# Kernel optimization log

Hardware: AMD Instinct MI355X
Metric: run time of the kernel (lower is better)

The kernel has to match this reference:

```python
import jax, jax.numpy as jnp
import numpy as np

B, T, H, S, A, E = 256, 64, 2048, 512, 64, 2048


def setup_inputs() -> dict:
    key = jax.random.key(0)
    ks = jax.random.split(key, 16)
    def w(k, shape, fan_in):
        return (jax.random.normal(k, shape, dtype=jnp.float32) / np.float32(np.sqrt(fan_in)))
    return {
        "prev_hidden": jax.random.normal(ks[0], (B, H), dtype=jnp.float32),
        "prev_state": jax.random.normal(ks[1], (B, S), dtype=jnp.float32),
        "actions": jax.random.normal(ks[2], (B, T, A), dtype=jnp.float32),
        "obs": jax.random.normal(ks[3], (B, T, E), dtype=jnp.float32),
        "prior_noise": jax.random.normal(ks[4], (B, T - 1, S), dtype=jnp.float32),
        "post_noise": jax.random.normal(ks[5], (B, T - 1, S), dtype=jnp.float32),
        # project_state_action: Linear(A+S -> H), stored [in, out]
        "W_sa": w(ks[6], (S + A, H), S + A), "b_sa": jnp.zeros((H,), jnp.float32),
        # GRUCell weights in torch layout [3H, in]
        "W_ih": w(ks[7], (3 * H, H), H), "W_hh": w(ks[8], (3 * H, H), H),
        "b_ih": jnp.zeros((3 * H,), jnp.float32), "b_hh": jnp.zeros((3 * H,), jnp.float32),
        # project_hidden_action: Linear(H+A -> H)
        "W_ha": w(ks[9], (H + A, H), H + A), "b_ha": jnp.zeros((H,), jnp.float32),
        # prior: Linear(H -> 2S)
        "W_prior": w(ks[10], (H, 2 * S), H), "b_prior": jnp.zeros((2 * S,), jnp.float32),
        # project_hidden_obs: Linear(H+E -> H)
        "W_ho": w(ks[11], (H + E, H), H + E), "b_ho": jnp.zeros((H,), jnp.float32),
        # posterior: Linear(H -> 2S)
        "W_post": w(ks[12], (H, 2 * S), H), "b_post": jnp.zeros((2 * S,), jnp.float32),
        "stop": 0,
    }


def reference(prev_hidden, prev_state, actions, obs, prior_noise, post_noise,
              W_sa, b_sa, W_ih, W_hh, b_ih, b_hh, W_ha, b_ha,
              W_prior, b_prior, W_ho, b_ho, W_post, b_post, stop):
    relu = jax.nn.relu

    def gru(x, h):
        gi = x @ W_ih.T + b_ih  # [B, 3H]
        gh = h @ W_hh.T + b_hh
        ir, iz, inn = jnp.split(gi, 3, axis=-1)
        hr, hz, hn = jnp.split(gh, 3, axis=-1)
        r = jax.nn.sigmoid(ir + hr)
        z = jax.nn.sigmoid(iz + hz)
        n = jnp.tanh(inn + r * hn)
        return (1.0 - z) * n + z * h

    def step(carry, xs):
        h, s = carry  # h: [B,H] hidden, s: [B,S] posterior state (obs is given)
        a, o, pn, qn = xs
        sa = relu(jnp.concatenate([s, a], axis=-1) @ W_sa + b_sa)
        h = gru(sa, h)
        ha = relu(jnp.concatenate([h, a], axis=-1) @ W_ha + b_ha)
        pm, plv = jnp.split(ha @ W_prior + b_prior, 2, axis=-1)
        ps = pm + jnp.exp(jax.nn.softplus(plv)) * pn  # prior rsample
        ho = relu(jnp.concatenate([h, o], axis=-1) @ W_ho + b_ho)
        qm, qlv = jnp.split(ho @ W_post + b_post, 2, axis=-1)
        qs = qm + jnp.exp(jax.nn.softplus(qlv)) * qn  # posterior rsample
        return (h, qs), (h, ps, qs, pm, plv, qm, qlv)

    Tm1 = actions.shape[1] - 1
    xs = (jnp.swapaxes(actions[:, :Tm1], 0, 1),
          jnp.swapaxes(obs[:, :Tm1], 0, 1),
          jnp.swapaxes(prior_noise, 0, 1),
          jnp.swapaxes(post_noise, 0, 1))
    _, ys = jax.lax.scan(step, (prev_hidden, prev_state), xs)
    hs, ps, qs, pm, plv, qm, qlv = (jnp.swapaxes(y, 0, 1) for y in ys)
    hiddens = jnp.concatenate([prev_hidden[:, None, :], hs], axis=1)       # [B, T, H]
    prior_states = jnp.concatenate([prev_state[:, None, :], ps], axis=1)   # [B, T, S]
    posterior_states = jnp.concatenate([prev_state[:, None, :], qs], axis=1)
    return (hiddens, prior_states, posterior_states, pm, plv, qm, qlv)
```

## Files before the change

kernel.cpp:

```cpp
#include <hip/hip_runtime.h>


typedef __attribute__((ext_vector_type(8))) short bf16x8;
typedef __attribute__((ext_vector_type(4))) float f32x4;
typedef __attribute__((ext_vector_type(4))) short s16x4;

#define DEVI static __device__ __forceinline__

DEVI float bf2f(short s) { union { float f; unsigned u; } v; v.u = ((unsigned)(unsigned short)s) << 16; return v.f; }
DEVI short f2bf(float f) {
  union { float f; unsigned u; } v; v.f = f;
  unsigned r = v.u + 0x7FFFu + ((v.u >> 16) & 1u);
  return (short)(r >> 16);
}

#define Bsz 256
#define Tsz 64
#define Hsz 2048
#define Ssz 512
#define Asz 64
#define Esz 2048
#define TM1 63

#define OUT_PS  33554432L
#define OUT_QS  41943040L
#define OUT_PM  50331648L
#define OUT_PLV 58589184L
#define OUT_QM  66846720L
#define OUT_QLV 75104256L

struct GArg {
  const short* A; const short* Bt; const float* bias; const short* Ci;
  float* oF; short* oB;
  int lda, ldb, ldoF, ldoB; long ldci, pstride;
};

template<int HASBIAS, int HASCI, int RELU, int OUTF, int OUTB>
__global__ __launch_bounds__(256) void gemm_bt(GArg g0, GArg g1, int kcK) {
  const int gemm = blockIdx.z & 1;
  const GArg g = gemm ? g1 : g0;
  const short* __restrict__ Ag = g.A;
  const short* __restrict__ Bg = g.Bt;
  __shared__ __align__(16) short As[2][8192];
  __shared__ __align__(16) short Bs[2][8192];
  const int tid = threadIdx.x;
  const int w = tid >> 6, l = tid & 63;
  const int bm0 = blockIdx.y << 7, bn0 = blockIdx.x << 7;
  const int fc = l & 15, fh = l >> 4;
  const int wr = (w >> 1) << 6, wc = (w & 1) << 6;
  const int rx = fc & 7;
  const int srccol = ((l & 7) ^ ((l >> 3) & 7)) << 3;
  long aoff[4], boff[4];
#pragma unroll
  for (int i = 0; i < 4; ++i) {
    const int row = (((i << 2) + w) << 3) + (l >> 3);
    aoff[i] = (long)(bm0 + row) * g.lda + srccol;
    boff[i] = (long)(bn0 + row) * g.ldb + srccol;
  }
  f32x4 acc[4][4];
#pragma unroll
  for (int i = 0; i < 4; ++i)
#pragma unroll
    for (int j = 0; j < 4; ++j) acc[i][j] = f32x4{0.f, 0.f, 0.f, 0.f};

  auto STAGE = [&](int kt, int buf) {
#pragma unroll
    for (int i = 0; i < 4; ++i) {
      const int ib = ((i << 2) + w) << 10;
      __builtin_amdgcn_global_load_lds(
          (const __attribute__((address_space(1))) void*)(Ag + aoff[i] + (kt << 6)),
          (__attribute__((address_space(3))) void*)((char*)&As[buf][0] + ib), 16, 0, 0);
      __builtin_amdgcn_global_load_lds(
          (const __attribute__((address_space(1))) void*)(Bg + boff[i] + (kt << 6)),
          (__attribute__((address_space(3))) void*)((char*)&Bs[buf][0] + ib), 16, 0, 0);
    }
  };
  auto COMPUTE = [&](int buf) {
#pragma unroll
    for (int kk = 0; kk < 2; ++kk) {
      bf16x8 af[4], bb[4];
#pragma unroll
      for (int mi = 0; mi < 4; ++mi)
        af[mi] = *(const bf16x8*)&As[buf][(wr + (mi << 4) + fc) * 64 + ((((kk << 2) + fh) ^ rx) << 3)];
#pragma unroll
      for (int ni = 0; ni < 4; ++ni)
        bb[ni] = *(const bf16x8*)&Bs[buf][(wc + (ni << 4) + fc) * 64 + ((((kk << 2) + fh) ^ rx) << 3)];
#pragma unroll
      for (int mi = 0; mi < 4; ++mi)
#pragma unroll
        for (int ni = 0; ni < 4; ++ni)
          acc[mi][ni] = __builtin_amdgcn_mfma_f32_16x16x32_bf16(af[mi], bb[ni], acc[mi][ni], 0, 0, 0);
    }
  };

  const int nk = kcK >> 6;
  STAGE(0, 0);
  for (int kt = 0; kt < nk - 1; ++kt) {
    STAGE(kt + 1, (kt + 1) & 1);
    asm volatile("s_waitcnt vmcnt(8)" ::: "memory");
    __builtin_amdgcn_s_barrier();
    __builtin_amdgcn_sched_barrier(0);
    COMPUTE(kt & 1);
    asm volatile("s_waitcnt lgkmcnt(0)" ::: "memory");
    __builtin_amdgcn_s_barrier();
  }
  asm volatile("s_waitcnt vmcnt(0)" ::: "memory");
  __builtin_amdgcn_s_barrier();
  __builtin_amdgcn_sched_barrier(0);
  COMPUTE((nk - 1) & 1);

#pragma unroll
  for (int mi = 0; mi < 4; ++mi) {
#pragma unroll
    for (int ni = 0; ni < 4; ++ni) {
      const int n = bn0 + wc + (ni << 4) + fc;
      float bv = 0.f;
      if (HASBIAS) bv = g.bias[n];
#pragma unroll
      for (int r = 0; r < 4; ++r) {
        const int m = bm0 + wr + (mi << 4) + (fh << 2) + r;
        float v = acc[mi][ni][r] + bv;
        if (HASCI) v += bf2f(g.Ci[(long)m * g.ldci + n]);
        if (RELU) v = fmaxf(v, 0.f);
        if (OUTF) g.oF[(long)m * g.ldoF + n] = v;
        if (OUTB) g.oB[(long)m * g.ldoB + n] = f2bf(v);
      }
    }
  }
}

__global__ __launch_bounds__(256) void gigh_gru(
    const short* __restrict__ sa, const short* __restrict__ hb_in,
    const short* __restrict__ Wih, const short* __restrict__ Whh,
    const float* __restrict__ b_ih, const float* __restrict__ b_hh,
    const float* __restrict__ hold, float* __restrict__ hnew,
    short* __restrict__ hb_out) {
  __shared__ __align__(16) short AsS[2][4096];
  __shared__ __align__(16) short AsH[2][4096];
  __shared__ __align__(16) short BsI[2][6144];
  __shared__ __align__(16) short BsH[2][6144];
  const int tid = threadIdx.x;
  const int w = tid >> 6, l = tid & 63;
  const int bm0 = blockIdx.y << 6;
  const int bn0 = blockIdx.x * 96;
  const int fc = l & 15, fh = l >> 4;
  const int wr = (w >> 1) << 5;
  const int wn = (w & 1) * 48;
  const int rx = fc & 7;
  const int srccol = ((l & 7) ^ ((l >> 3) & 7)) << 3;

  long aoff[2], boff[3];
#pragma unroll
  for (int i = 0; i < 2; ++i) {
    const int row = (((i << 2) + w) << 3) + (l >> 3);
    aoff[i] = (long)(bm0 + row) * Hsz + srccol;
  }
#pragma unroll
  for (int i = 0; i < 3; ++i) {
    const int row = (((i << 2) + w) << 3) + (l >> 3);
    boff[i] = (long)(bn0 + row) * Hsz + srccol;
  }

  f32x4 acc_i[2][3], acc_h[2][3];
#pragma unroll
  for (int i = 0; i < 2; ++i)
#pragma unroll
    for (int j = 0; j < 3; ++j) { acc_i[i][j] = f32x4{0.f,0.f,0.f,0.f}; acc_h[i][j] = f32x4{0.f,0.f,0.f,0.f}; }

  auto STAGE = [&](int kt, int buf) {
#pragma unroll
    for (int i = 0; i < 2; ++i) {
      const int ib = ((i << 2) + w) << 10;
      __builtin_amdgcn_global_load_lds(
          (const __attribute__((address_space(1))) void*)(sa + aoff[i] + (kt << 6)),
          (__attribute__((address_space(3))) void*)((char*)&AsS[0][0] + (buf << 13) + ib), 16, 0, 0);
      __builtin_amdgcn_global_load_lds(
          (const __attribute__((address_space(1))) void*)(hb_in + aoff[i] + (kt << 6)),
          (__attribute__((address_space(3))) void*)((char*)&AsH[0][0] + (buf << 13) + ib), 16, 0, 0);
    }
#pragma unroll
    for (int i = 0; i < 3; ++i) {
      const int ib = ((i << 2) + w) << 10;
      __builtin_amdgcn_global_load_lds(
          (const __attribute__((address_space(1))) void*)(Wih + boff[i] + (kt << 6)),
          (__attribute__((address_space(3))) void*)((char*)&BsI[0][0] + buf * 12288 + ib), 16, 0, 0);
      __builtin_amdgcn_global_load_lds(
          (const __attribute__((address_space(1))) void*)(Whh + boff[i] + (kt << 6)),
          (__attribute__((address_space(3))) void*)((char*)&BsH[0][0] + buf * 12288 + ib), 16, 0, 0);
    }
  };
  auto COMPUTE = [&](int buf) {
#pragma unroll
    for (int kk = 0; kk < 2; ++kk) {
      const int sw = (((kk << 2) + fh) ^ rx) << 3;
      bf16x8 as_[2], ah_[2], bi_[3], bh_[3];
#pragma unroll
      for (int mi = 0; mi < 2; ++mi) {
        as_[mi] = *(const bf16x8*)&AsS[buf][(wr + (mi << 4) + fc) * 64 + sw];
        ah_[mi] = *(const bf16x8*)&AsH[buf][(wr + (mi << 4) + fc) * 64 + sw];
      }
#pragma unroll
      for (int ni = 0; ni < 3; ++ni) {
        bi_[ni] = *(const bf16x8*)&BsI[buf][(wn + (ni << 4) + fc) * 64 + sw];
        bh_[ni] = *(const bf16x8*)&BsH[buf][(wn + (ni << 4) + fc) * 64 + sw];
      }
#pragma unroll
      for (int mi = 0; mi < 2; ++mi)
#pragma unroll
        for (int ni = 0; ni < 3; ++ni) {
          acc_i[mi][ni] = __builtin_amdgcn_mfma_f32_16x16x32_bf16(as_[mi], bi_[ni], acc_i[mi][ni], 0, 0, 0);
          acc_h[mi][ni] = __builtin_amdgcn_mfma_f32_16x16x32_bf16(ah_[mi], bh_[ni], acc_h[mi][ni], 0, 0, 0);
        }
    }
  };

  const int nk = Hsz >> 6;
  STAGE(0, 0);
  for (int kt = 0; kt < nk - 1; ++kt) {
    STAGE(kt + 1, (kt + 1) & 1);
    asm volatile("s_waitcnt vmcnt(10)" ::: "memory");
    __builtin_amdgcn_s_barrier();
    __builtin_amdgcn_sched_barrier(0);
    COMPUTE(kt & 1);
    asm volatile("s_waitcnt lgkmcnt(0)" ::: "memory");
    __builtin_amdgcn_s_barrier();
  }
  asm volatile("s_waitcnt vmcnt(0)" ::: "memory");
  __builtin_amdgcn_s_barrier();
  __builtin_amdgcn_sched_barrier(0);
  COMPUTE((nk - 1) & 1);

  const int j = (((int)blockIdx.x << 1) + (w & 1)) * 16 + fc;
  const float bir = b_ih[j],            bhr = b_hh[j];
  const float biz = b_ih[Hsz + j],      bhz = b_hh[Hsz + j];
  const float bin = b_ih[2 * Hsz + j],  bhn = b_hh[2 * Hsz + j];
#pragma unroll
  for (int mi = 0; mi < 2; ++mi) {
#pragma unroll
    for (int r = 0; r < 4; ++r) {
      const int m = bm0 + wr + (mi << 4) + (fh << 2) + r;
      const float ir = acc_i[mi][0][r] + bir, hr = acc_h[mi][0][r] + bhr;
      const float iz = acc_i[mi][1][r] + biz, hz = acc_h[mi][1][r] + bhz;
      const float in_ = acc_i[mi][2][r] + bin, hn = acc_h[mi][2][r] + bhn;
      const float rg = 1.f / (1.f + expf(-(ir + hr)));
      const float zg = 1.f / (1.f + expf(-(iz + hz)));
      const float ng = tanhf(in_ + rg * hn);
      const float hv = (1.f - zg) * ng + zg * hold[(long)m * (Tsz * Hsz) + j];
      hnew[(long)m * (Tsz * Hsz) + j] = hv;
      hb_out[m * Hsz + j] = f2bf(hv);
    }
  }
}

__global__ __launch_bounds__(256) void haho64(
    const short* __restrict__ A, const short* __restrict__ B0,
    const short* __restrict__ B1, const short* __restrict__ Ci0,
    const short* __restrict__ Ci1, long ldci,
    short* __restrict__ o0, short* __restrict__ o1) {
  const int z = blockIdx.z;
  const short* __restrict__ Bg = z ? B1 : B0;
  const short* __restrict__ Ci = z ? Ci1 : Ci0;
  short* __restrict__ o = z ? o1 : o0;
  __shared__ __align__(16) short As[2][4096];
  __shared__ __align__(16) short Bs[2][4096];
  const int tid = threadIdx.x;
  const int w = tid >> 6, l = tid & 63;
  const int bm0 = blockIdx.y << 6, bn0 = blockIdx.x << 6;
  const int fc = l & 15, fh = l >> 4;
  const int wr = (w >> 1) << 5, wc = (w & 1) << 5;
  const int rx = fc & 7;
  const int srccol = ((l & 7) ^ ((l >> 3) & 7)) << 3;

  long aoff[2], boff[2];
#pragma unroll
  for (int i = 0; i < 2; ++i) {
    const int row = (((i << 2) + w) << 3) + (l >> 3);
    aoff[i] = (long)(bm0 + row) * Hsz + srccol;
    boff[i] = (long)(bn0 + row) * Hsz + srccol;
  }

  f32x4 acc[2][2];
#pragma unroll
  for (int i = 0; i < 2; ++i)
#pragma unroll
    for (int j = 0; j < 2; ++j) acc[i][j] = f32x4{0.f, 0.f, 0.f, 0.f};

  auto STAGE = [&](int kt, int buf) {
#pragma unroll
    for (int i = 0; i < 2; ++i) {
      const int ib = ((i << 2) + w) << 10;
      __builtin_amdgcn_global_load_lds(
          (const __attribute__((address_space(1))) void*)(A + aoff[i] + (kt << 6)),
          (__attribute__((address_space(3))) void*)((char*)&As[buf][0] + ib), 16, 0, 0);
      __builtin_amdgcn_global_load_lds(
          (const __attribute__((address_space(1))) void*)(Bg + boff[i] + (kt << 6)),
          (__attribute__((address_space(3))) void*)((char*)&Bs[buf][0] + ib), 16, 0, 0);
    }
  };
  auto COMPUTE = [&](int buf) {
#pragma unroll
    for (int kk = 0; kk < 2; ++kk) {
      const int sw = (((kk << 2) + fh) ^ rx) << 3;
      bf16x8 af[2], bb[2];
#pragma unroll
      for (int mi = 0; mi < 2; ++mi)
        af[mi] = *(const bf16x8*)&As[buf][(wr + (mi << 4) + fc) * 64 + sw];
#pragma unroll
      for (int ni = 0; ni < 2; ++ni)
        bb[ni] = *(const bf16x8*)&Bs[buf][(wc + (ni << 4) + fc) * 64 + sw];
#pragma unroll
      for (int mi = 0; mi < 2; ++mi)
#pragma unroll
        for (int ni = 0; ni < 2; ++ni)
          acc[mi][ni] = __builtin_amdgcn_mfma_f32_16x16x32_bf16(af[mi], bb[ni], acc[mi][ni], 0, 0, 0);
    }
  };

  const int nk = Hsz >> 6;
  STAGE(0, 0);
  for (int kt = 0; kt < nk - 1; ++kt) {
    STAGE(kt + 1, (kt + 1) & 1);
    asm volatile("s_waitcnt vmcnt(4)" ::: "memory");
    __builtin_amdgcn_s_barrier();
    __builtin_amdgcn_sched_barrier(0);
    COMPUTE(kt & 1);
    asm volatile("s_waitcnt lgkmcnt(0)" ::: "memory");
    __builtin_amdgcn_s_barrier();
  }
  asm volatile("s_waitcnt vmcnt(0)" ::: "memory");
  __builtin_amdgcn_s_barrier();
  __builtin_amdgcn_sched_barrier(0);
  COMPUTE((nk - 1) & 1);

#pragma unroll
  for (int mi = 0; mi < 2; ++mi) {
#pragma unroll
    for (int ni = 0; ni < 2; ++ni) {
      const int n = bn0 + wc + (ni << 4) + fc;
#pragma unroll
      for (int r = 0; r < 4; ++r) {
        const int m = bm0 + wr + (mi << 4) + (fh << 2) + r;
        const float v = acc[mi][ni][r] + bf2f(Ci[(long)m * ldci + n]);
        o[(long)m * Hsz + n] = f2bf(fmaxf(v, 0.f));
      }
    }
  }
}

__global__ __launch_bounds__(256) void prpo_sample64(
    const short* __restrict__ A0, const short* __restrict__ A1,
    const short* __restrict__ B0, const short* __restrict__ B1,
    const float* __restrict__ bi0, const float* __restrict__ bi1,
    const float* __restrict__ n0, const float* __restrict__ n1,
    float* __restrict__ out, short* __restrict__ sb, int t) {
  const int z = blockIdx.z;
  const short* __restrict__ A = z ? A1 : A0;
  const short* __restrict__ Bg = z ? B1 : B0;
  const float* __restrict__ bias = z ? bi1 : bi0;
  const float* __restrict__ noise = z ? n1 : n0;
  const long oS = z ? OUT_QS : OUT_PS, oM = z ? OUT_QM : OUT_PM, oLV = z ? OUT_QLV : OUT_PLV;
  __shared__ __align__(16) short As[2][4096];
  __shared__ __align__(16) short Bs[2][4096];
  const int tid = threadIdx.x;
  const int w = tid >> 6, l = tid & 63;
  const int bm0 = blockIdx.y << 6, bn0 = blockIdx.x << 6;
  const int fc = l & 15, fh = l >> 4;
  const int wr = (w >> 1) << 5, wc = (w & 1) << 5;
  const int rx = fc & 7;
  const int srccol = ((l & 7) ^ ((l >> 3) & 7)) << 3;

  long aoff[2], boff[2];
#pragma unroll
  for (int i = 0; i < 2; ++i) {
    const int row = (((i << 2) + w) << 3) + (l >> 3);
    aoff[i] = (long)(bm0 + row) * Hsz + srccol;
    boff[i] = (long)(bn0 + row) * Hsz + srccol;
  }

  f32x4 acc[2][2];
#pragma unroll
  for (int i = 0; i < 2; ++i)
#pragma unroll
    for (int j = 0; j < 2; ++j) acc[i][j] = f32x4{0.f, 0.f, 0.f, 0.f};

  auto STAGE = [&](int kt, int buf) {
#pragma unroll
    for (int i = 0; i < 2; ++i) {
      const int ib = ((i << 2) + w) << 10;
      __builtin_amdgcn_global_load_lds(
          (const __attribute__((address_space(1))) void*)(A + aoff[i] + (kt << 6)),
          (__attribute__((address_space(3))) void*)((char*)&As[buf][0] + ib), 16, 0, 0);
      __builtin_amdgcn_global_load_lds(
          (const __attribute__((address_space(1))) void*)(Bg + boff[i] + (kt << 6)),
          (__attribute__((address_space(3))) void*)((char*)&Bs[buf][0] + ib), 16, 0, 0);
    }
  };
  auto COMPUTE = [&](int buf) {
#pragma unroll
    for (int kk = 0; kk < 2; ++kk) {
      const int sw = (((kk << 2) + fh) ^ rx) << 3;
      bf16x8 af[2], bb[2];
#pragma unroll
      for (int mi = 0; mi < 2; ++mi)
        af[mi] = *(const bf16x8*)&As[buf][(wr + (mi << 4) + fc) * 64 + sw];
#pragma unroll
      for (int ni = 0; ni < 2; ++ni)
        bb[ni] = *(const bf16x8*)&Bs[buf][(wc + (ni << 4) + fc) * 64 + sw];
#pragma unroll
      for (int mi = 0; mi < 2; ++mi)
#pragma unroll
        for (int ni = 0; ni < 2; ++ni)
          acc[mi][ni] = __builtin_amdgcn_mfma_f32_16x16x32_bf16(af[mi], bb[ni], acc[mi][ni], 0, 0, 0);
    }
  };

  const int nk = Hsz >> 6;
  STAGE(0, 0);
  for (int kt = 0; kt < nk - 1; ++kt) {
    STAGE(kt + 1, (kt + 1) & 1);
    asm volatile("s_waitcnt vmcnt(4)" ::: "memory");
    __builtin_amdgcn_s_barrier();
    __builtin_amdgcn_sched_barrier(0);
    COMPUTE(kt & 1);
    asm volatile("s_waitcnt lgkmcnt(0)" ::: "memory");
    __builtin_amdgcn_s_barrier();
  }
  asm volatile("s_waitcnt vmcnt(0)" ::: "memory");
  __builtin_amdgcn_s_barrier();
  __builtin_amdgcn_sched_barrier(0);
  COMPUTE((nk - 1) & 1);

  const int j = (((bn0 + wc) >> 5) << 4) + fc;
  const float bm_ = bias[j], blv = bias[512 + j];
#pragma unroll
  for (int mi = 0; mi < 2; ++mi) {
#pragma unroll
    for (int r = 0; r < 4; ++r) {
      const int b = bm0 + wr + (mi << 4) + (fh << 2) + r;
      const float mv = acc[mi][0][r] + bm_;
      const float lv = acc[mi][1][r] + blv;
      const long noff = ((long)b * TM1 + t) * Ssz + j;
      const float sv = mv + (1.f + expf(lv)) * noise[noff];
      out[oS + (long)b * (Tsz * Ssz) + (long)(t + 1) * Ssz + j] = sv;
      out[oM + noff] = mv;
      out[oLV + noff] = lv;
      if (z) sb[b * Ssz + j] = f2bf(sv);
    }
  }
}

__global__ void conv_f2b(const float* __restrict__ src, short* __restrict__ dst, long n) {
  long i = ((long)blockIdx.x * 256 + threadIdx.x) * 4;
  const long stride = (long)gridDim.x * 1024;
  for (; i < n; i += stride) {
    float4 v = *(const float4*)(src + i);
    s16x4 o;
    o[0] = f2bf(v.x); o[1] = f2bf(v.y); o[2] = f2bf(v.z); o[3] = f2bf(v.w);
    *(s16x4*)(dst + i) = o;
  }
}

__global__ void conv_perm48(const float* __restrict__ src, short* __restrict__ dst) {
  const long e = ((long)blockIdx.x * 256 + threadIdx.x) * 4;
  const int np = (int)(e >> 11), col = (int)(e & 2047);
  const int u = np / 48, rem = np - u * 48;
  const int g = rem >> 4, jlo = rem & 15;
  const long srow = ((long)g << 11) + u * 16 + jlo;
  float4 v = *(const float4*)&src[srow * 2048 + col];
  s16x4 o;
  o[0] = f2bf(v.x); o[1] = f2bf(v.y); o[2] = f2bf(v.z); o[3] = f2bf(v.w);
  *(s16x4*)&dst[e] = o;
}

template<int PERM>
__global__ void transp(const float* __restrict__ src, short* __restrict__ dst,
                       int srcld, int k0, int K, int N) {
  __shared__ float t[32][33];
  const int tx = threadIdx.x, ty = threadIdx.y;
  const int kb = blockIdx.y << 5, nb = blockIdx.x << 5;
#pragma unroll
  for (int i = ty; i < 32; i += 8)
    t[i][tx] = src[(long)(k0 + kb + i) * srcld + nb + tx];
  __syncthreads();
#pragma unroll
  for (int i = ty; i < 32; i += 8) {
    int n = nb + i, drow = n;
    if (PERM) { const int j = n & 511, lvb = n >> 9; drow = ((j >> 4) << 5) | (lvb << 4) | (j & 15); }
    dst[(long)drow * K + kb + tx] = f2bf(t[tx][i]);
  }
}

__global__ void init_kernel(const float* __restrict__ ph, const float* __restrict__ ps,
                            float* __restrict__ out, short* __restrict__ hb, short* __restrict__ sb) {
  const int idx = blockIdx.x * 256 + threadIdx.x;
  const int b = idx >> 11, n = idx & 2047;
  const float h = ph[idx];
  out[(long)b * (Tsz * Hsz) + n] = h;
  hb[idx] = f2bf(h);
  if (n < Ssz) {
    const int sidx = b * Ssz + n;
    const float s = ps[sidx];
    out[OUT_PS + (long)b * (Tsz * Ssz) + n] = s;
    out[OUT_QS + (long)b * (Tsz * Ssz) + n] = s;
    sb[sidx] = f2bf(s);
  }
}

static GArg mk(const short* A, int lda, const short* Bt, int ldb, const float* bias,
               const short* Ci, long ldci, float* oF, int ldoF, long pstride,
               short* oB, int ldoB) {
  GArg g; g.A = A; g.Bt = Bt; g.bias = bias; g.Ci = Ci; g.ldci = ldci;
  g.oF = oF; g.oB = oB; g.lda = lda; g.ldb = ldb; g.ldoF = ldoF; g.ldoB = ldoB;
  g.pstride = pstride;
  return g;
}

extern "C" void kernel_launch(void* const* d_in, const int* in_sizes, int n_in,
                              void* d_out, int out_size, void* d_ws, size_t ws_size,
                              hipStream_t stream) {
  const float* prev_hidden = (const float*)d_in[0];
  const float* prev_state  = (const float*)d_in[1];
  const float* actions     = (const float*)d_in[2];
  const float* obs         = (const float*)d_in[3];
  const float* prior_noise = (const float*)d_in[4];
  const float* post_noise  = (const float*)d_in[5];
  const float* W_sa = (const float*)d_in[6];
  const float* b_sa = (const float*)d_in[7];
  const float* W_ih = (const float*)d_in[8];
  const float* W_hh = (const float*)d_in[9];
  const float* b_ih = (const float*)d_in[10];
  const float* b_hh = (const float*)d_in[11];
  const float* W_ha = (const float*)d_in[12];
  const float* b_ha = (const float*)d_in[13];
  const float* W_prior = (const float*)d_in[14];
  const float* b_prior = (const float*)d_in[15];
  const float* W_ho = (const float*)d_in[16];
  const float* b_ho = (const float*)d_in[17];
  const float* W_post = (const float*)d_in[18];
  const float* b_post = (const float*)d_in[19];
  float* out = (float*)d_out;

  char* p = (char*)d_ws;
  auto alloc = [&](size_t bytes) { char* r = p; p += (bytes + 255) & ~(size_t)255; return r; };
  short* Wih_p   = (short*)alloc(3L * Hsz * Hsz * 2);
  short* Whh_p   = (short*)alloc(3L * Hsz * Hsz * 2);
  short* Wt_sa_s = (short*)alloc((long)Hsz * Ssz * 2);
  short* Wt_sa_a = (short*)alloc((long)Hsz * Asz * 2);
  short* Wt_ha_h = (short*)alloc((long)Hsz * Hsz * 2);
  short* Wt_ha_a = (short*)alloc((long)Hsz * Asz * 2);
  short* Wt_ho_h = (short*)alloc((long)Hsz * Hsz * 2);
  short* Wt_ho_o = (short*)alloc((long)Hsz * Esz * 2);
  short* Wt_pr   = (short*)alloc(2L * Ssz * Hsz * 2);
  short* Wt_po   = (short*)alloc(2L * Ssz * Hsz * 2);
  short* obs_b   = (short*)alloc((long)Bsz * Tsz * Esz * 2);
  short* act_b   = (short*)alloc((long)Bsz * Tsz * Asz * 2);
  short* a_pre   = (short*)alloc((long)Bsz * Tsz * Hsz * 2);
  short* ha_a    = (short*)alloc((long)Bsz * Tsz * Hsz * 2);
  short* ho_o    = (short*)alloc((long)Bsz * Tsz * Hsz * 2);
  short* s_b     = (short*)alloc((long)Bsz * Ssz * 2);
  short* h_b1    = (short*)alloc((long)Bsz * Hsz * 2);
  short* h_b2    = (short*)alloc((long)Bsz * Hsz * 2);
  short* sa_b    = (short*)alloc((long)Bsz * Hsz * 2);
  short* ha_b    = (short*)alloc((long)Bsz * Hsz * 2);
  short* ho_b    = (short*)alloc((long)Bsz * Hsz * 2);
  (void)ws_size; (void)in_sizes; (void)n_in; (void)out_size;

  conv_f2b<<<4096, 256, 0, stream>>>(obs,  obs_b, (long)Bsz * Tsz * Esz);
  conv_f2b<<<1024, 256, 0, stream>>>(actions, act_b, (long)Bsz * Tsz * Asz);
  conv_perm48<<<12288, 256, 0, stream>>>(W_ih, Wih_p);
  conv_perm48<<<12288, 256, 0, stream>>>(W_hh, Whh_p);

  dim3 tb(32, 8);
  transp<0><<<dim3(Hsz / 32, Ssz / 32), tb, 0, stream>>>(W_sa, Wt_sa_s, Hsz, 0,   Ssz, Hsz);
  transp<0><<<dim3(Hsz / 32, Asz / 32), tb, 0, stream>>>(W_sa, Wt_sa_a, Hsz, Ssz, Asz, Hsz);
  transp<0><<<dim3(Hsz / 32, Hsz / 32), tb, 0, stream>>>(W_ha, Wt_ha_h, Hsz, 0,   Hsz, Hsz);
  transp<0><<<dim3(Hsz / 32, Asz / 32), tb, 0, stream>>>(W_ha, Wt_ha_a, Hsz, Hsz, Asz, Hsz);
  transp<0><<<dim3(Hsz / 32, Hsz / 32), tb, 0, stream>>>(W_ho, Wt_ho_h, Hsz, 0,   Hsz, Hsz);
  transp<0><<<dim3(Hsz / 32, Esz / 32), tb, 0, stream>>>(W_ho, Wt_ho_o, Hsz, Hsz, Esz, Hsz);
  transp<1><<<dim3(2 * Ssz / 32, Hsz / 32), tb, 0, stream>>>(W_prior, Wt_pr, 2 * Ssz, 0, Hsz, 2 * Ssz);
  transp<1><<<dim3(2 * Ssz / 32, Hsz / 32), tb, 0, stream>>>(W_post,  Wt_po, 2 * Ssz, 0, Hsz, 2 * Ssz);

  init_kernel<<<2048, 256, 0, stream>>>(prev_hidden, prev_state, out, h_b1, s_b);

  {
    GArg g0 = mk(act_b, Asz, Wt_sa_a, Asz, b_sa, nullptr, 0, nullptr, 0, 0, a_pre, Hsz);
    GArg g1 = mk(act_b, Asz, Wt_ha_a, Asz, b_ha, nullptr, 0, nullptr, 0, 0, ha_a, Hsz);
    gemm_bt<1, 0, 0, 0, 1><<<dim3(Hsz / 128, (Bsz * Tsz) / 128, 2), 256, 0, stream>>>(g0, g1, Asz);
  }
  {
    GArg g0 = mk(obs_b, Esz, Wt_ho_o, Esz, b_ho, nullptr, 0, nullptr, 0, 0, ho_o, Hsz);
    gemm_bt<1, 0, 0, 0, 1><<<dim3(Hsz / 128, (Bsz * Tsz) / 128, 1), 256, 0, stream>>>(g0, g0, Esz);
  }

  const long ldPre = (long)Tsz * Hsz;
  for (int t = 0; t < TM1; ++t) {
    short* hp = (t & 1) ? h_b2 : h_b1;
    short* hn = (t & 1) ? h_b1 : h_b2;
    {
      GArg g0 = mk(s_b, Ssz, Wt_sa_s, Ssz, nullptr, a_pre + (long)t * Hsz, ldPre,
                   nullptr, 0, 0, sa_b, Hsz);
      gemm_bt<0, 1, 1, 0, 1><<<dim3(16, 2, 1), 256, 0, stream>>>(g0, g0, Ssz);
    }
    gigh_gru<<<dim3(64, 4, 1), 256, 0, stream>>>(
        sa_b, hp, Wih_p, Whh_p, b_ih, b_hh,
        out + (long)t * Hsz, out + (long)(t + 1) * Hsz, hn);
    haho64<<<dim3(32, 4, 2), 256, 0, stream>>>(
        hn, Wt_ha_h, Wt_ho_h, ha_a + (long)t * Hsz, ho_o + (long)t * Hsz, ldPre,
        ha_b, ho_b);
    prpo_sample64<<<dim3(16, 4, 2), 256, 0, stream>>>(
        ha_b, ho_b, Wt_pr, Wt_po, b_prior, b_post,
        prior_noise, post_noise, out, s_b, t);
  }
}
```

Baseline: 7.419 ms.

## Replace per-step recurrent GEMMs with single-wave tiled kernels for more blocks

After: 6.444 ms (median of 2 runs). 1.15x faster.

```diff
diff --git a/kernel.cpp b/kernel.cpp
--- a/kernel.cpp
+++ b/kernel.cpp
@@ -34,6 +34,196 @@
   float* oF; short* oB;
   int lda, ldb, ldoF, ldoB; long ldci, pstride;
 };
+
+template<int MI>
+__global__ __launch_bounds__(64) void gemm_w(
+    const short* __restrict__ A0, const short* __restrict__ A1,
+    const short* __restrict__ B0, const short* __restrict__ B1,
+    const short* __restrict__ Ci0, const short* __restrict__ Ci1, long ldci,
+    short* __restrict__ o0, short* __restrict__ o1,
+    int lda, int ldb, int ldo, int nk) {
+  const int z = blockIdx.z;
+  const short* __restrict__ A  = z ? A1 : A0;
+  const short* __restrict__ Bg = z ? B1 : B0;
+  const short* __restrict__ Ci = z ? Ci1 : Ci0;
+  short* __restrict__ o = z ? o1 : o0;
+  __shared__ __align__(16) short As[2][MI * 1024];
+  __shared__ __align__(16) short Bs[2][2048];
+  const int l = threadIdx.x;
+  const int bm0 = blockIdx.y * (MI * 16), bn0 = blockIdx.x << 5;
+  const int fc = l & 15, fh = l >> 4, rx = fc & 7;
+  const int srccol = ((l & 7) ^ ((l >> 3) & 7)) << 3;
+
+  long aoff[2 * MI], boff[4];
+#pragma unroll
+  for (int i = 0; i < 2 * MI; ++i)
+    aoff[i] = (long)(bm0 + (i << 3) + (l >> 3)) * lda + srccol;
+#pragma unroll
+  for (int i = 0; i < 4; ++i)
+    boff[i] = (long)(bn0 + (i << 3) + (l >> 3)) * ldb + srccol;
+
+  f32x4 acc[MI][2];
+#pragma unroll
+  for (int i = 0; i < MI; ++i)
+#pragma unroll
+    for (int j = 0; j < 2; ++j) acc[i][j] = f32x4{0.f, 0.f, 0.f, 0.f};
+
+  auto STAGE = [&](int kt, int buf) {
+#pragma unroll
+    for (int i = 0; i < 2 * MI; ++i)
+      __builtin_amdgcn_global_load_lds(
+          (const __attribute__((address_space(1))) void*)(A + aoff[i] + (kt << 6)),
+          (__attribute__((address_space(3))) void*)((char*)&As[buf][0] + (i << 10)), 16, 0, 0);
+#pragma unroll
+    for (int i = 0; i < 4; ++i)
+      __builtin_amdgcn_global_load_lds(
+          (const __attribute__((address_space(1))) void*)(Bg + boff[i] + (kt << 6)),
+          (__attribute__((address_space(3))) void*)((char*)&Bs[buf][0] + (i << 10)), 16, 0, 0);
+  };
+  auto COMPUTE = [&](int buf) {
+#pragma unroll
+    for (int kk = 0; kk < 2; ++kk) {
+      const int sw = (((kk << 2) + fh) ^ rx) << 3;
+      bf16x8 af[MI], bb[2];
+#pragma unroll
+      for (int mi = 0; mi < MI; ++mi)
+        af[mi] = *(const bf16x8*)&As[buf][((mi << 4) + fc) * 64 + sw];
+#pragma unroll
+      for (int ni = 0; ni < 2; ++ni)
+        bb[ni] = *(const bf16x8*)&Bs[buf][((ni << 4) + fc) * 64 + sw];
+#pragma unroll
+      for (int mi = 0; mi < MI; ++mi)
+#pragma unroll
+        for (int ni = 0; ni < 2; ++ni)
+          acc[mi][ni] = __builtin_amdgcn_mfma_f32_16x16x32_bf16(af[mi], bb[ni], acc[mi][ni], 0, 0, 0);
+    }
+  };
+
+  STAGE(0, 0);
+  for (int kt = 0; kt < nk; ++kt) {
+    if (kt + 1 < nk) {
+      STAGE(kt + 1, (kt + 1) & 1);
+      asm volatile("s_waitcnt vmcnt(%0)" :: "i"(2 * MI + 4) : "memory");
+    } else {
+      asm volatile("s_waitcnt vmcnt(0)" ::: "memory");
+    }
+    __builtin_amdgcn_sched_barrier(0);
+    COMPUTE(kt & 1);
+    asm volatile("s_waitcnt lgkmcnt(0)" ::: "memory");
+    __builtin_amdgcn_sched_barrier(0);
+  }
+
+#pragma unroll
+  for (int mi = 0; mi < MI; ++mi) {
+#pragma unroll
+    for (int ni = 0; ni < 2; ++ni) {
+      const int n = bn0 + (ni << 4) + fc;
+#pragma unroll
+      for (int r = 0; r < 4; ++r) {
+        const int m = bm0 + (mi << 4) + (fh << 2) + r;
+        const float v = acc[mi][ni][r] + bf2f(Ci[(long)m * ldci + n]);
+        o[(long)m * ldo + n] = f2bf(fmaxf(v, 0.f));
+      }
+    }
+  }
+}
+
+__global__ __launch_bounds__(64) void prpo_sample_w(
+    const short* __restrict__ A0, const short* __restrict__ A1,
+    const short* __restrict__ B0, const short* __restrict__ B1,
+    const float* __restrict__ bi0, const float* __restrict__ bi1,
+    const float* __restrict__ n0, const float* __restrict__ n1,
+    float* __restrict__ out, short* __restrict__ sb, int t) {
+  const int z = blockIdx.z;
+  const short* __restrict__ A  = z ? A1 : A0;
+  const short* __restrict__ Bg = z ? B1 : B0;
+  const float* __restrict__ bias = z ? bi1 : bi0;
+  const float* __restrict__ noise = z ? n1 : n0;
+  const long oS = z ? OUT_QS : OUT_PS, oM = z ? OUT_QM : OUT_PM, oLV = z ? OUT_QLV : OUT_PLV;
+  __shared__ __align__(16) short As[2][2048];
+  __shared__ __align__(16) short Bs[2][2048];
+  const int l = threadIdx.x;
+  const int bm0 = blockIdx.y << 5, bn0 = blockIdx.x << 5;
+  const int fc = l & 15, fh = l >> 4, rx = fc & 7;
+  const int srccol = ((l & 7) ^ ((l >> 3) & 7)) << 3;
+
+  long aoff[4], boff[4];
+#pragma unroll
+  for (int i = 0; i < 4; ++i) {
+    const int row = (i << 3) + (l >> 3);
+    aoff[i] = (long)(bm0 + row) * Hsz + srccol;
+    boff[i] = (long)(bn0 + row) * Hsz + srccol;
+  }
+
+  f32x4 acc[2][2];
+#pragma unroll
+  for (int i = 0; i < 2; ++i)
+#pragma unroll
+    for (int j = 0; j < 2; ++j) acc[i][j] = f32x4{0.f, 0.f, 0.f, 0.f};
+
+  auto STAGE = [&](int kt, int buf) {
+#pragma unroll
+    for (int i = 0; i < 4; ++i) {
+      __builtin_amdgcn_global_load_lds(
+          (const __attribute__((address_space(1))) void*)(A + aoff[i] + (kt << 6)),
+          (__attribute__((address_space(3))) void*)((char*)&As[buf][0] + (i << 10)), 16, 0, 0);
+      __builtin_amdgcn_global_load_lds(
+          (const __attribute__((address_space(1))) void*)(Bg + boff[i] + (kt << 6)),
+          (__attribute__((address_space(3))) void*)((char*)&Bs[buf][0] + (i << 10)), 16, 0, 0);
+    }
+  };
+  auto COMPUTE = [&](int buf) {
+#pragma unroll
+    for (int kk = 0; kk < 2; ++kk) {
+      const int sw = (((kk << 2) + fh) ^ rx) << 3;
+      bf16x8 af[2], bb[2];
+#pragma unroll
+      for (int mi = 0; mi < 2; ++mi)
+        af[mi] = *(const bf16x8*)&As[buf][((mi << 4) + fc) * 64 + sw];
+#pragma unroll
+      for (int ni = 0; ni < 2; ++ni)
+        bb[ni] = *(const bf16x8*)&Bs[buf][((ni << 4) + fc) * 64 + sw];
+#pragma unroll
+      for (int mi = 0; mi < 2; ++mi)
+#pragma unroll
+        for (int ni = 0; ni < 2; ++ni)
+          acc[mi][ni] = __builtin_amdgcn_mfma_f32_16x16x32_bf16(af[mi], bb[ni], acc[mi][ni], 0, 0, 0);
+    }
+  };
+
+  const int nk = Hsz >> 6;
+  STAGE(0, 0);
+  for (int kt = 0; kt < nk; ++kt) {
+    if (kt + 1 < nk) {
+      STAGE(kt + 1, (kt + 1) & 1);
+      asm volatile("s_waitcnt vmcnt(8)" ::: "memory");
+    } else {
+      asm volatile("s_waitcnt vmcnt(0)" ::: "memory");
+    }
+    __builtin_amdgcn_sched_barrier(0);
+    COMPUTE(kt & 1);
+    asm volatile("s_waitcnt lgkmcnt(0)" ::: "memory");
+    __builtin_amdgcn_sched_barrier(0);
+  }
+
+  const int j = ((bn0 >> 5) << 4) + fc;
+  const float bm_ = bias[j], blv = bias[512 + j];
+#pragma unroll
+  for (int mi = 0; mi < 2; ++mi) {
+#pragma unroll
+    for (int r = 0; r < 4; ++r) {
+      const int b = bm0 + (mi << 4) + (fh << 2) + r;
+      const float mv = acc[mi][0][r] + bm_;
+      const float lv = acc[mi][1][r] + blv;
+      const long noff = ((long)b * TM1 + t) * Ssz + j;
+      const float sv = mv + (1.f + expf(lv)) * noise[noff];
+      out[oS + (long)b * (Tsz * Ssz) + (long)(t + 1) * Ssz + j] = sv;
+      out[oM + noff] = mv;
+      out[oLV + noff] = lv;
+      if (z) sb[b * Ssz + j] = f2bf(sv);
+    }
+  }
+}
 
 template<int HASBIAS, int HASCI, int RELU, int OUTF, int OUTB>
 __global__ __launch_bounds__(256) void gemm_bt(GArg g0, GArg g1, int kcK) {
@@ -248,203 +438,6 @@
       const float hv = (1.f - zg) * ng + zg * hold[(long)m * (Tsz * Hsz) + j];
       hnew[(long)m * (Tsz * Hsz) + j] = hv;
       hb_out[m * Hsz + j] = f2bf(hv);
-    }
-  }
-}
-
-__global__ __launch_bounds__(256) void haho64(
-    const short* __restrict__ A, const short* __restrict__ B0,
-    const short* __restrict__ B1, const short* __restrict__ Ci0,
-    const short* __restrict__ Ci1, long ldci,
-    short* __restrict__ o0, short* __restrict__ o1) {
-  const int z = blockIdx.z;
-  const short* __restrict__ Bg = z ? B1 : B0;
-  const short* __restrict__ Ci = z ? Ci1 : Ci0;
-  short* __restrict__ o = z ? o1 : o0;
-  __shared__ __align__(16) short As[2][4096];
-  __shared__ __align__(16) short Bs[2][4096];
-  const int tid = threadIdx.x;
-  const int w = tid >> 6, l = tid & 63;
-  const int bm0 = blockIdx.y << 6, bn0 = blockIdx.x << 6;
-  const int fc = l & 15, fh = l >> 4;
-  const int wr = (w >> 1) << 5, wc = (w & 1) << 5;
-  const int rx = fc & 7;
-  const int srccol = ((l & 7) ^ ((l >> 3) & 7)) << 3;
-
-  long aoff[2], boff[2];
-#pragma unroll
-  for (int i = 0; i < 2; ++i) {
-    const int row = (((i << 2) + w) << 3) + (l >> 3);
-    aoff[i] = (long)(bm0 + row) * Hsz + srccol;
-    boff[i] = (long)(bn0 + row) * Hsz + srccol;
-  }
-
-  f32x4 acc[2][2];
-#pragma unroll
-  for (int i = 0; i < 2; ++i)
-#pragma unroll
-    for (int j = 0; j < 2; ++j) acc[i][j] = f32x4{0.f, 0.f, 0.f, 0.f};
-
-  auto STAGE = [&](int kt, int buf) {
-#pragma unroll
-    for (int i = 0; i < 2; ++i) {
-      const int ib = ((i << 2) + w) << 10;
-      __builtin_amdgcn_global_load_lds(
-          (const __attribute__((address_space(1))) void*)(A + aoff[i] + (kt << 6)),
-          (__attribute__((address_space(3))) void*)((char*)&As[buf][0] + ib), 16, 0, 0);
-      __builtin_amdgcn_global_load_lds(
-          (const __attribute__((address_space(1))) void*)(Bg + boff[i] + (kt << 6)),
-          (__attribute__((address_space(3))) void*)((char*)&Bs[buf][0] + ib), 16, 0, 0);
-    }
-  };
-  auto COMPUTE = [&](int buf) {
-#pragma unroll
-    for (int kk = 0; kk < 2; ++kk) {
-      const int sw = (((kk << 2) + fh) ^ rx) << 3;
-      bf16x8 af[2], bb[2];
-#pragma unroll
-      for (int mi = 0; mi < 2; ++mi)
-        af[mi] = *(const bf16x8*)&As[buf][(wr + (mi << 4) + fc) * 64 + sw];
-#pragma unroll
-      for (int ni = 0; ni < 2; ++ni)
-        bb[ni] = *(const bf16x8*)&Bs[buf][(wc + (ni << 4) + fc) * 64 + sw];
-#pragma unroll
-      for (int mi = 0; mi < 2; ++mi)
-#pragma unroll
-        for (int ni = 0; ni < 2; ++ni)
-          acc[mi][ni] = __builtin_amdgcn_mfma_f32_16x16x32_bf16(af[mi], bb[ni], acc[mi][ni], 0, 0, 0);
-    }
-  };
-
-  const int nk = Hsz >> 6;
-  STAGE(0, 0);
-  for (int kt = 0; kt < nk - 1; ++kt) {
-    STAGE(kt + 1, (kt + 1) & 1);
-    asm volatile("s_waitcnt vmcnt(4)" ::: "memory");
-    __builtin_amdgcn_s_barrier();
-    __builtin_amdgcn_sched_barrier(0);
-    COMPUTE(kt & 1);
-    asm volatile("s_waitcnt lgkmcnt(0)" ::: "memory");
-    __builtin_amdgcn_s_barrier();
-  }
-  asm volatile("s_waitcnt vmcnt(0)" ::: "memory");
-  __builtin_amdgcn_s_barrier();
-  __builtin_amdgcn_sched_barrier(0);
-  COMPUTE((nk - 1) & 1);
-
-#pragma unroll
-  for (int mi = 0; mi < 2; ++mi) {
-#pragma unroll
-    for (int ni = 0; ni < 2; ++ni) {
-      const int n = bn0 + wc + (ni << 4) + fc;
-#pragma unroll
-      for (int r = 0; r < 4; ++r) {
-        const int m = bm0 + wr + (mi << 4) + (fh << 2) + r;
-        const float v = acc[mi][ni][r] + bf2f(Ci[(long)m * ldci + n]);
-        o[(long)m * Hsz + n] = f2bf(fmaxf(v, 0.f));
-      }
-    }
-  }
-}
-
-__global__ __launch_bounds__(256) void prpo_sample64(
-    const short* __restrict__ A0, const short* __restrict__ A1,
-    const short* __restrict__ B0, const short* __restrict__ B1,
-    const float* __restrict__ bi0, const float* __restrict__ bi1,
-    const float* __restrict__ n0, const float* __restrict__ n1,
-    float* __restrict__ out, short* __restrict__ sb, int t) {
-  const int z = blockIdx.z;
-  const short* __restrict__ A = z ? A1 : A0;
-  const short* __restrict__ Bg = z ? B1 : B0;
-  const float* __restrict__ bias = z ? bi1 : bi0;
-  const float* __restrict__ noise = z ? n1 : n0;
-  const long oS = z ? OUT_QS : OUT_PS, oM = z ? OUT_QM : OUT_PM, oLV = z ? OUT_QLV : OUT_PLV;
-  __shared__ __align__(16) short As[2][4096];
-  __shared__ __align__(16) short Bs[2][4096];
-  const int tid = threadIdx.x;
-  const int w = tid >> 6, l = tid & 63;
-  const int bm0 = blockIdx.y << 6, bn0 = blockIdx.x << 6;
-  const int fc = l & 15, fh = l >> 4;
-  const int wr = (w >> 1) << 5, wc = (w & 1) << 5;
-  const int rx = fc & 7;
-  const int srccol = ((l & 7) ^ ((l >> 3) & 7)) << 3;
-
-  long aoff[2], boff[2];
-#pragma unroll
-  for (int i = 0; i < 2; ++i) {
-    const int row = (((i << 2) + w) << 3) + (l >> 3);
-    aoff[i] = (long)(bm0 + row) * Hsz + srccol;
-    boff[i] = (long)(bn0 + row) * Hsz + srccol;
-  }
-
-  f32x4 acc[2][2];
-#pragma unroll
-  for (int i = 0; i < 2; ++i)
-#pragma unroll
-    for (int j = 0; j < 2; ++j) acc[i][j] = f32x4{0.f, 0.f, 0.f, 0.f};
-
-  auto STAGE = [&](int kt, int buf) {
-#pragma unroll
-    for (int i = 0; i < 2; ++i) {
-      const int ib = ((i << 2) + w) << 10;
-      __builtin_amdgcn_global_load_lds(
-          (const __attribute__((address_space(1))) void*)(A + aoff[i] + (kt << 6)),
-          (__attribute__((address_space(3))) void*)((char*)&As[buf][0] + ib), 16, 0, 0);
-      __builtin_amdgcn_global_load_lds(
-          (const __attribute__((address_space(1))) void*)(Bg + boff[i] + (kt << 6)),
-          (__attribute__((address_space(3))) void*)((char*)&Bs[buf][0] + ib), 16, 0, 0);
-    }
-  };
-  auto COMPUTE = [&](int buf) {
-#pragma unroll
-    for (int kk = 0; kk < 2; ++kk) {
-      const int sw = (((kk << 2) + fh) ^ rx) << 3;
-      bf16x8 af[2], bb[2];
-#pragma unroll
-      for (int mi = 0; mi < 2; ++mi)
-        af[mi] = *(const bf16x8*)&As[buf][(wr + (mi << 4) + fc) * 64 + sw];
-#pragma unroll
-      for (int ni = 0; ni < 2; ++ni)
-        bb[ni] = *(const bf16x8*)&Bs[buf][(wc + (ni << 4) + fc) * 64 + sw];
-#pragma unroll
-      for (int mi = 0; mi < 2; ++mi)
-#pragma unroll
-        for (int ni = 0; ni < 2; ++ni)
-          acc[mi][ni] = __builtin_amdgcn_mfma_f32_16x16x32_bf16(af[mi], bb[ni], acc[mi][ni], 0, 0, 0);
-    }
-  };
-
-  const int nk = Hsz >> 6;
-  STAGE(0, 0);
-  for (int kt = 0; kt < nk - 1; ++kt) {
-    STAGE(kt + 1, (kt + 1) & 1);
-    asm volatile("s_waitcnt vmcnt(4)" ::: "memory");
-    __builtin_amdgcn_s_barrier();
-    __builtin_amdgcn_sched_barrier(0);
-    COMPUTE(kt & 1);
-    asm volatile("s_waitcnt lgkmcnt(0)" ::: "memory");
-    __builtin_amdgcn_s_barrier();
-  }
-  asm volatile("s_waitcnt vmcnt(0)" ::: "memory");
-  __builtin_amdgcn_s_barrier();
-  __builtin_amdgcn_sched_barrier(0);
-  COMPUTE((nk - 1) & 1);
-
-  const int j = (((bn0 + wc) >> 5) << 4) + fc;
-  const float bm_ = bias[j], blv = bias[512 + j];
-#pragma unroll
-  for (int mi = 0; mi < 2; ++mi) {
-#pragma unroll
-    for (int r = 0; r < 4; ++r) {
-      const int b = bm0 + wr + (mi << 4) + (fh << 2) + r;
-      const float mv = acc[mi][0][r] + bm_;
-      const float lv = acc[mi][1][r] + blv;
-      const long noff = ((long)b * TM1 + t) * Ssz + j;
-      const float sv = mv + (1.f + expf(lv)) * noise[noff];
-      out[oS + (long)b * (Tsz * Ssz) + (long)(t + 1) * Ssz + j] = sv;
-      out[oM + noff] = mv;
-      out[oLV + noff] = lv;
-      if (z) sb[b * Ssz + j] = f2bf(sv);
     }
   }
 }
@@ -596,18 +589,16 @@
   for (int t = 0; t < TM1; ++t) {
     short* hp = (t & 1) ? h_b2 : h_b1;
     short* hn = (t & 1) ? h_b1 : h_b2;
-    {
-      GArg g0 = mk(s_b, Ssz, Wt_sa_s, Ssz, nullptr, a_pre + (long)t * Hsz, ldPre,
-                   nullptr, 0, 0, sa_b, Hsz);
-      gemm_bt<0, 1, 1, 0, 1><<<dim3(16, 2, 1), 256, 0, stream>>>(g0, g0, Ssz);
-    }
+    gemm_w<4><<<dim3(64, 4, 1), 64, 0, stream>>>(
+        s_b, s_b, Wt_sa_s, Wt_sa_s, a_pre + (long)t * Hsz, a_pre + (long)t * Hsz,
+        ldPre, sa_b, sa_b, Ssz, Ssz, Hsz, Ssz / 64);
     gigh_gru<<<dim3(64, 4, 1), 256, 0, stream>>>(
         sa_b, hp, Wih_p, Whh_p, b_ih, b_hh,
         out + (long)t * Hsz, out + (long)(t + 1) * Hsz, hn);
-    haho64<<<dim3(32, 4, 2), 256, 0, stream>>>(
-        hn, Wt_ha_h, Wt_ho_h, ha_a + (long)t * Hsz, ho_o + (long)t * Hsz, ldPre,
-        ha_b, ho_b);
-    prpo_sample64<<<dim3(16, 4, 2), 256, 0, stream>>>(
+    gemm_w<4><<<dim3(64, 4, 2), 64, 0, stream>>>(
+        hn, hn, Wt_ha_h, Wt_ho_h, ha_a + (long)t * Hsz, ho_o + (long)t * Hsz,
+        ldPre, ha_b, ho_b, Hsz, Hsz, Hsz, Hsz / 64);
+    prpo_sample_w<<<dim3(32, 8, 2), 64, 0, stream>>>(
         ha_b, ho_b, Wt_pr, Wt_po, b_prior, b_post,
         prior_noise, post_noise, out, s_b, t);
   }
```
